# Kernel optimization log

Hardware: AMD Instinct MI355X
Metric: run time of the kernel (lower is better)

The kernel has to match this reference:

```python
import jax, jax.numpy as jnp
import numpy as np
import math

NUM_HEADS = 16
HEAD_DIM = 64
DIM = 1024
IO_SLOTS = 16
NEG_INF = 1.0e9


def _alibi_slopes(num_heads):
    # slopes = ratio**i for i in 1..n, ratio = 2**(-8/n)
    ratio = 2.0 ** (-8.0 / num_heads)
    return jnp.array([ratio ** i for i in range(1, num_heads + 1)], dtype=jnp.float32)


def setup_inputs() -> dict:
    key = jax.random.key(0)
    ks = jax.random.split(key, 7)
    B, S, D = 2, 2048, DIM
    x = jax.random.normal(ks[0], (B, S, D), dtype=jnp.float32)
    is_getchar = jax.random.uniform(ks[1], (B, S), dtype=jnp.float32)
    is_putchar = jax.random.uniform(ks[2], (B, S), dtype=jnp.float32)
    scale = 0.02
    wq = jax.random.normal(ks[3], (D, NUM_HEADS * HEAD_DIM), dtype=jnp.float32) * scale
    wk = jax.random.normal(ks[4], (D, NUM_HEADS * HEAD_DIM), dtype=jnp.float32) * scale
    wv = jax.random.normal(ks[5], (D, NUM_HEADS * HEAD_DIM), dtype=jnp.float32) * scale
    wo = jax.random.normal(ks[6], (NUM_HEADS * HEAD_DIM, D), dtype=jnp.float32) * scale
    return {"x": x, "is_getchar": is_getchar, "is_putchar": is_putchar,
            "wq": wq, "wk": wk, "wv": wv, "wo": wo}


def reference(x, is_getchar, is_putchar, wq, wk, wv, wo):
    B, S, D = x.shape
    H, hd = NUM_HEADS, HEAD_DIM
    io_start = D - IO_SLOTS

    q = (x @ wq).reshape(B, S, H, hd)
    k = (x @ wk).reshape(B, S, H, hd)
    v = (x @ wv).reshape(B, S, H, hd)

    # scores[b,h,i,j] = q . k / sqrt(hd)
    scores = jnp.einsum("bihd,bjhd->bhij", q, k) / math.sqrt(hd)

    # standard ALiBi bias: -slope * (i - j), causal masked
    positions = jnp.arange(S)
    dist = (positions[:, None] - positions[None, :]).astype(jnp.float32)  # [S,S] = i - j
    slopes = _alibi_slopes(H)  # [H]
    bias = -slopes[:, None, None] * dist  # [H,S,S]
    causal = jnp.triu(jnp.ones((S, S), dtype=jnp.float32), k=1)
    bias = bias - causal * NEG_INF
    scores = scores + bias[None]

    # targeted read-head bias on head 0: -slope0 * |target - j|
    read_anchor = x[..., io_start + 0]  # [B,S]
    read_offset = x[..., io_start + 1]  # [B,S]
    target = read_anchor + 1.0 + read_offset  # [B,S]
    read_bias = -slopes[0] * jnp.abs(target[..., None] - positions.astype(jnp.float32))  # [B,S,S]
    head0 = jnp.where(is_getchar[:, None, :, None] > 0.5, read_bias[:, None], scores[:, :1])
    scores = scores.at[:, :1].set(head0)

    attn = jax.nn.softmax(scores, axis=-1)
    attn_out = jnp.einsum("bhij,bjhd->bihd", attn, v).reshape(B, S, H * hd)
    output = x + attn_out @ wo

    # I/O state updates (last 16 channels)
    output = output.at[..., io_start + 1].add(is_getchar)   # read_offset += getchar
    output = output.at[..., io_start + 3].add(is_putchar)   # write_offset += putchar
    output = output.at[..., io_start + 13].set(is_putchar)  # output_ready = putchar
    return output
```

## Files before the change

kernel.cpp:

```cpp
#include <hip/hip_runtime.h>
#include <hip/hip_bf16.h>

typedef __hip_bfloat16 bf16;
typedef __attribute__((ext_vector_type(8))) short short8;
typedef __attribute__((ext_vector_type(4))) short short4v;
typedef __attribute__((ext_vector_type(4))) float f32x4;

#define MFMA16(a, b, c) __builtin_amdgcn_mfma_f32_16x16x32_bf16((a), (b), (c), 0, 0, 0)

#if __has_builtin(__builtin_amdgcn_mfma_f32_16x16x16bf16_1k)
#define MFMA_PV(a, b, c) __builtin_amdgcn_mfma_f32_16x16x16bf16_1k((a), (b), (c), 0, 0, 0)
#elif __has_builtin(__builtin_amdgcn_mfma_f32_16x16x16_bf16)
#define MFMA_PV(a, b, c) __builtin_amdgcn_mfma_f32_16x16x16_bf16((a), (b), (c), 0, 0, 0)
#else
static __device__ __forceinline__ f32x4 mfma_pv_asm(short4v a, short4v b, f32x4 c) {
    f32x4 d;
    asm volatile("v_mfma_f32_16x16x16_bf16 %0, %1, %2, %3"
                 : "=&v"(d) : "v"(a), "v"(b), "v"(c));
    return d;
}
#define MFMA_PV(a, b, c) mfma_pv_asm((a), (b), (c))
#endif

static __device__ __forceinline__ void gload_lds16(const bf16* g, bf16* l) {
    __builtin_amdgcn_global_load_lds((const __attribute__((address_space(1))) void*)g,
                                     (__attribute__((address_space(3))) void*)l, 16, 0, 0);
}

__global__ __launch_bounds__(256) void prep_kernel(
    const float* __restrict__ x, bf16* __restrict__ Xb,
    const float* __restrict__ wq, const float* __restrict__ wk,
    const float* __restrict__ wv, const float* __restrict__ wo,
    bf16* __restrict__ WqkvT, bf16* __restrict__ WoT) {
    __shared__ bf16 tile[64][65];
    int bidx = blockIdx.x;
    if (bidx >= 1024) {
        int i = ((bidx - 1024) * 256 + threadIdx.x) * 4;
        float4 v = *(const float4*)(x + i);
        union { bf16 h4[4]; uint2 u; } p;
        p.h4[0] = __float2bfloat16(v.x);
        p.h4[1] = __float2bfloat16(v.y);
        p.h4[2] = __float2bfloat16(v.z);
        p.h4[3] = __float2bfloat16(v.w);
        *(uint2*)(Xb + i) = p.u;
        return;
    }
    int mat = bidx >> 8;
    int t   = bidx & 255;
    int tn  = t >> 4, tk = t & 15;
    const float* src = (mat == 0) ? wq : (mat == 1) ? wk : (mat == 2) ? wv : wo;
    bf16* dst = (mat < 3) ? (WqkvT + (size_t)mat * 1024 * 1024) : WoT;
    int tx = threadIdx.x & 63, ty = threadIdx.x >> 6;
    int k0 = tk * 64, n0 = tn * 64;
#pragma unroll
    for (int p = 0; p < 16; ++p) {
        int r = p * 4 + ty;
        tile[r][tx] = __float2bfloat16(src[(size_t)(k0 + r) * 1024 + n0 + tx]);
    }
    __syncthreads();
#pragma unroll
    for (int p = 0; p < 16; ++p) {
        int r = p * 4 + ty;
        dst[(size_t)(n0 + r) * 1024 + k0 + tx] = tile[tx][r];
    }
}

__global__ __launch_bounds__(256) void gemm_qkv_kernel(
    const bf16* __restrict__ A, const bf16* __restrict__ Bt,
    bf16* __restrict__ QK, bf16* __restrict__ Vt) {
    const int K = 1024;
    int bm = blockIdx.x, bn = blockIdx.y;
    __shared__ bf16 As[128 * 32];
    __shared__ bf16 Bs[128 * 32];
    int tid = threadIdx.x;
    int lane = tid & 63, w = tid >> 6;
    int wm = (w >> 1) * 64, wn = (w & 1) * 64;
    int q4 = lane >> 4, li = lane & 15;
    int srow = tid >> 2, sc = (tid & 3) * 8;

    const bf16* Ag = A + (size_t)(bm * 128 + srow) * K + sc;
    const bf16* Bg = Bt + (size_t)(bn * 128 + srow) * K + sc;
    bf16* Asl = As + tid * 8;
    bf16* Asl2 = As + 2048 + tid * 8;
    bf16* Bsl = Bs + tid * 8;
    bf16* Bsl2 = Bs + 2048 + tid * 8;

    f32x4 acc[4][4];
#pragma unroll
    for (int mt = 0; mt < 4; ++mt)
#pragma unroll
        for (int nt = 0; nt < 4; ++nt) acc[mt][nt] = (f32x4){0.f, 0.f, 0.f, 0.f};

    for (int k0 = 0; k0 < K; k0 += 32) {
        __syncthreads();
        gload_lds16(Ag + k0, Asl);
        gload_lds16(Ag + 64 * K + k0, Asl2);
        gload_lds16(Bg + k0, Bsl);
        gload_lds16(Bg + 64 * K + k0, Bsl2);
        __syncthreads();
        short8 af[4], bfb[4];
#pragma unroll
        for (int mt = 0; mt < 4; ++mt)
            af[mt] = *(const short8*)(As + (wm + mt * 16 + li) * 32 + q4 * 8);
#pragma unroll
        for (int nt = 0; nt < 4; ++nt)
            bfb[nt] = *(const short8*)(Bs + (wn + nt * 16 + li) * 32 + q4 * 8);
#pragma unroll
        for (int mt = 0; mt < 4; ++mt)
#pragma unroll
            for (int nt = 0; nt < 4; ++nt)
                acc[mt][nt] = MFMA16(af[mt], bfb[nt], acc[mt][nt]);
    }

    int rowb = bm * 128 + wm;
    if (bn < 16) {
        float qs = (bn < 8) ? 0.1803368801111204f : 1.0f;
#pragma unroll
        for (int mt = 0; mt < 4; ++mt) {
#pragma unroll
            for (int nt = 0; nt < 4; ++nt) {
                int col = bn * 128 + wn + nt * 16 + li;
#pragma unroll
                for (int r = 0; r < 4; ++r) {
                    int row = rowb + mt * 16 + q4 * 4 + r;
                    QK[(size_t)row * 2048 + col] = __float2bfloat16(acc[mt][nt][r] * qs);
                }
            }
        }
    } else {
#pragma unroll
        for (int mt = 0; mt < 4; ++mt) {
            int sbase = rowb + mt * 16 + q4 * 4;
            int b = sbase >> 11, s = sbase & 2047;
#pragma unroll
            for (int nt = 0; nt < 4; ++nt) {
                int n = bn * 128 + wn + nt * 16 + li - 2048;
                int h = n >> 6, d = n & 63;
                union { bf16 h4[4]; uint2 u; } pk;
#pragma unroll
                for (int r = 0; r < 4; ++r) pk.h4[r] = __float2bfloat16(acc[mt][nt][r]);
                *(uint2*)(Vt + (size_t)((b * 16 + h) * 64 + d) * 2048 + s) = pk.u;
            }
        }
    }
}

__global__ __launch_bounds__(256, 3) void attn_kernel(
    const bf16* __restrict__ QK, const bf16* __restrict__ Vt,
    const float* __restrict__ x, const float* __restrict__ gch,
    bf16* __restrict__ AO) {
    const int S = 2048;
    int idx = blockIdx.x;
    int ti, h, b;
    if (idx < 64) { h = 0; b = idx & 1; ti = idx >> 1; }
    else {
        int i2 = idx - 64;
        int row = i2 / 30;
        int j = i2 - row * 30;
        ti = 31 - row; h = 1 + (j >> 1); b = j & 1;
    }
    int i0 = ti * 64;
    int tid = threadIdx.x, lane = tid & 63, w = tid >> 6;
    int q4 = lane >> 4, li = lane & 15;

    __shared__ __align__(16) char smem[36864];
    bf16* KsB = (bf16*)smem;
    bf16* VsB = (bf16*)(smem + 18432);
    float* Ored = (float*)smem;
    float* lsumBuf = (float*)(smem + 17408);

    short8 qf[4][2];
#pragma unroll
    for (int it = 0; it < 4; ++it) {
        const bf16* qp = QK + (size_t)(b * S + i0 + it * 16 + li) * 2048 + h * 64 + q4 * 8;
        qf[it][0] = *(const short8*)(qp);
        qf[it][1] = *(const short8*)(qp + 32);
    }

    const float L2E = 1.4426950408889634f;
    float slope = exp2f(-0.5f * (float)(h + 1));
    float sl1 = slope * L2E;
    const float slope0_1 = 0.70710678118654752f * L2E;

    float tgt[4]; int gcm[4];
    if (h == 0) {
#pragma unroll
        for (int it = 0; it < 4; ++it) {
            size_t ix = (size_t)(b * S + i0 + it * 16 + li);
            gcm[it] = gch[ix] > 0.5f ? 1 : 0;
            tgt[it] = x[ix * 1024 + 1008] + 1.0f + x[ix * 1024 + 1009];
        }
    } else {
#pragma unroll
        for (int it = 0; it < 4; ++it) { gcm[it] = 0; tgt[it] = 0.f; }
    }

    float lsum[4] = {0.f, 0.f, 0.f, 0.f};
    f32x4 o[4][4];
#pragma unroll
    for (int it = 0; it < 4; ++it)
#pragma unroll
        for (int dt = 0; dt < 4; ++dt) o[it][dt] = (f32x4){0.f, 0.f, 0.f, 0.f};

    int srow = tid >> 3, scv = (tid & 7) * 8;
    const bf16* Kg = QK + (size_t)(b * S + srow) * 2048 + 1024 + h * 64 + scv;
    const bf16* Vg = Vt + (size_t)((b * 16 + h) * 64 + srow) * 2048 + scv;

    int ntiles = (h == 0) ? (S / 64) : (ti + 1);

    {
        uint4 kv0 = *(const uint4*)(Kg);
        uint4 kv1 = *(const uint4*)(Kg + (size_t)32 * 2048);
        uint4 vv0 = *(const uint4*)(Vg);
        uint4 vv1 = *(const uint4*)(Vg + (size_t)32 * 2048);
        *(uint4*)(KsB + srow * 72 + scv) = kv0;
        *(uint4*)(KsB + (srow + 32) * 72 + scv) = kv1;
        *(uint4*)(VsB + srow * 72 + scv) = vv0;
        *(uint4*)(VsB + (srow + 32) * 72 + scv) = vv1;
    }
    __syncthreads();

    int cur = 0;
    for (int jt = 0; jt < ntiles; ++jt) {
        int j0 = jt * 64;
        uint4 nk0, nk1, nv0, nv1;
        bool pref = (jt + 1 < ntiles);
        if (pref) {
            int jn = j0 + 64;
            nk0 = *(const uint4*)(Kg + (size_t)jn * 2048);
            nk1 = *(const uint4*)(Kg + (size_t)(jn + 32) * 2048);
            nv0 = *(const uint4*)(Vg + jn);
            nv1 = *(const uint4*)(Vg + (size_t)32 * 2048 + jn);
        }
        const bf16* Ks = KsB + cur * 4608;
        const bf16* Vs = VsB + cur * 4608;

        short8 kf0 = *(const short8*)(Ks + (w * 16 + li) * 72 + q4 * 8);
        short8 kf1 = *(const short8*)(Ks + (w * 16 + li) * 72 + 32 + q4 * 8);
        f32x4 sAcc[4];
#pragma unroll
        for (int it = 0; it < 4; ++it) {
            f32x4 z = (f32x4){0.f, 0.f, 0.f, 0.f};
            z = MFMA16(kf0, qf[it][0], z);
            z = MFMA16(kf1, qf[it][1], z);
            sAcc[it] = z;
        }

        float jbase = (float)(j0 + w * 16 + q4 * 4);
        int maskable = (jt >= ti);
        short4v pf[4];
#pragma unroll
        for (int it = 0; it < 4; ++it) {
            float fi = (float)(i0 + it * 16 + li);
            float d0 = jbase - fi;
            union { bf16 hh[4]; short4v v; } pu;
#pragma unroll
            for (int r = 0; r < 4; ++r) {
                float dj = d0 + (float)r;
                float s = fmaf(sl1, dj, sAcc[it][r]);
                float p;
                if (h == 0) {
                    float jj = jbase + (float)r;
                    float sg = -slope0_1 * fabsf(tgt[it] - jj);
                    s = gcm[it] ? sg : s;
                    bool msk = (!gcm[it]) && (dj > 0.f);
                    p = msk ? 0.f : exp2f(s);
                } else {
                    p = exp2f(s);
                    if (maskable && dj > 0.f) p = 0.f;
                }
                lsum[it] += p;
                pu.hh[r] = __float2bfloat16(p);
            }
            pf[it] = pu.v;
        }

#pragma unroll
        for (int dt = 0; dt < 4; ++dt) {
            short4v vf = *(const short4v*)(Vs + (dt * 16 + li) * 72 + w * 16 + q4 * 4);
#pragma unroll
            for (int it = 0; it < 4; ++it)
                o[it][dt] = MFMA_PV(pf[it], vf, o[it][dt]);
        }

        if (pref) {
            bf16* Kn = KsB + (cur ^ 1) * 4608;
            bf16* Vn = VsB + (cur ^ 1) * 4608;
            *(uint4*)(Kn + srow * 72 + scv) = nk0;
            *(uint4*)(Kn + (srow + 32) * 72 + scv) = nk1;
            *(uint4*)(Vn + srow * 72 + scv) = nv0;
            *(uint4*)(Vn + (srow + 32) * 72 + scv) = nv1;
        }
        __syncthreads();
        cur ^= 1;
    }

#pragma unroll
    for (int it = 0; it < 4; ++it) {
        lsum[it] += __shfl_xor(lsum[it], 16, 64);
        lsum[it] += __shfl_xor(lsum[it], 32, 64);
    }
    if (lane < 16) {
#pragma unroll
        for (int it = 0; it < 4; ++it) lsumBuf[w * 64 + it * 16 + lane] = lsum[it];
    }

    __syncthreads();
    if (w == 0) {
#pragma unroll
        for (int it = 0; it < 4; ++it)
#pragma unroll
            for (int dt = 0; dt < 4; ++dt)
#pragma unroll
                for (int r = 0; r < 4; ++r)
                    Ored[(it * 16 + q4 * 4 + r) * 68 + dt * 16 + li] = o[it][dt][r];
    }
    __syncthreads();
    if (w == 1) {
#pragma unroll
        for (int it = 0; it < 4; ++it)
#pragma unroll
            for (int dt = 0; dt < 4; ++dt)
#pragma unroll
                for (int r = 0; r < 4; ++r)
                    Ored[(it * 16 + q4 * 4 + r) * 68 + dt * 16 + li] += o[it][dt][r];
    }
    __syncthreads();
    if (w == 2) {
#pragma unroll
        for (int it = 0; it < 4; ++it)
#pragma unroll
            for (int dt = 0; dt < 4; ++dt)
#pragma unroll
                for (int r = 0; r < 4; ++r)
                    Ored[(it * 16 + q4 * 4 + r) * 68 + dt * 16 + li] += o[it][dt][r];
    }
    __syncthreads();
    if (w == 3) {
#pragma unroll
        for (int it = 0; it < 4; ++it)
#pragma unroll
            for (int dt = 0; dt < 4; ++dt)
#pragma unroll
                for (int r = 0; r < 4; ++r)
                    Ored[(it * 16 + q4 * 4 + r) * 68 + dt * 16 + li] += o[it][dt][r];
    }
    __syncthreads();

    int i = tid >> 2, dseg = (tid & 3) * 16;
    float ls = lsumBuf[0 * 64 + i] + lsumBuf[1 * 64 + i] + lsumBuf[2 * 64 + i] + lsumBuf[3 * 64 + i];
    float inv = 1.0f / ls;
    bf16* dst = AO + (size_t)(b * S + i0 + i) * 1024 + h * 64 + dseg;
    union { bf16 hh[16]; uint4 u[2]; } ou;
#pragma unroll
    for (int c = 0; c < 16; ++c)
        ou.hh[c] = __float2bfloat16(Ored[i * 68 + dseg + c] * inv);
    *(uint4*)(dst) = ou.u[0];
    *(uint4*)(dst + 8) = ou.u[1];
}

__global__ __launch_bounds__(256) void gemm_out_kernel(
    const bf16* __restrict__ A, const bf16* __restrict__ Bt,
    const float* __restrict__ x, float* __restrict__ out,
    const float* __restrict__ gch, const float* __restrict__ pch) {
    const int K = 1024;
    int bm = blockIdx.x, bn = blockIdx.y;
    __shared__ bf16 As[64 * 32];
    __shared__ bf16 Bs[128 * 32];
    int tid = threadIdx.x;
    int lane = tid & 63, w = tid >> 6;
    int wm = (w >> 1) * 32, wn = (w & 1) * 64;
    int q4 = lane >> 4, li = lane & 15;
    int srow = tid >> 2, sc = (tid & 3) * 8;

    const bf16* Ag = A + (size_t)(bm * 64 + srow) * K + sc;
    const bf16* Bg = Bt + (size_t)(bn * 128 + srow) * K + sc;
    bf16* Asl = As + tid * 8;
    bf16* Bsl = Bs + tid * 8;
    bf16* Bsl2 = Bs + 2048 + tid * 8;

    f32x4 acc[2][4];
#pragma unroll
    for (int mt = 0; mt < 2; ++mt)
#pragma unroll
        for (int nt = 0; nt < 4; ++nt) acc[mt][nt] = (f32x4){0.f, 0.f, 0.f, 0.f};

    for (int k0 = 0; k0 < K; k0 += 32) {
        __syncthreads();
        gload_lds16(Ag + k0, Asl);
        gload_lds16(Bg + k0, Bsl);
        gload_lds16(Bg + 64 * K + k0, Bsl2);
        __syncthreads();
        short8 af[2], bfb[4];
#pragma unroll
        for (int mt = 0; mt < 2; ++mt)
            af[mt] = *(const short8*)(As + (wm + mt * 16 + li) * 32 + q4 * 8);
#pragma unroll
        for (int nt = 0; nt < 4; ++nt)
            bfb[nt] = *(const short8*)(Bs + (wn + nt * 16 + li) * 32 + q4 * 8);
#pragma unroll
        for (int mt = 0; mt < 2; ++mt)
#pragma unroll
            for (int nt = 0; nt < 4; ++nt)
                acc[mt][nt] = MFMA16(af[mt], bfb[nt], acc[mt][nt]);
    }

#pragma unroll
    for (int mt = 0; mt < 2; ++mt) {
#pragma unroll
        for (int nt = 0; nt < 4; ++nt) {
            int col = bn * 128 + wn + nt * 16 + li;
#pragma unroll
            for (int r = 0; r < 4; ++r) {
                int row = bm * 64 + wm + mt * 16 + q4 * 4 + r;
                size_t idx = (size_t)row * 1024 + col;
                float v = x[idx] + acc[mt][nt][r];
                if (col == 1009) v += gch[row];
                else if (col == 1011) v += pch[row];
                else if (col == 1021) v = pch[row];
                out[idx] = v;
            }
        }
    }
}

extern "C" void kernel_launch(void* const* d_in, const int* in_sizes, int n_in,
                              void* d_out, int out_size, void* d_ws, size_t ws_size,
                              hipStream_t stream) {
    (void)in_sizes; (void)n_in; (void)out_size; (void)ws_size;
    const float* x   = (const float*)d_in[0];
    const float* gch = (const float*)d_in[1];
    const float* pch = (const float*)d_in[2];
    const float* wq  = (const float*)d_in[3];
    const float* wk  = (const float*)d_in[4];
    const float* wv  = (const float*)d_in[5];
    const float* wo  = (const float*)d_in[6];
    float* out = (float*)d_out;

    char* ws = (char*)d_ws;
    bf16* Xb    = (bf16*)(ws);
    bf16* WqkvT = (bf16*)(ws + (size_t)( 8 << 20));
    bf16* WoT   = (bf16*)(ws + (size_t)(14 << 20));
    bf16* QK    = (bf16*)(ws + (size_t)(16 << 20));
    bf16* Vt    = (bf16*)(ws + (size_t)(32 << 20));
    bf16* AO    = Xb;

    prep_kernel<<<5120, 256, 0, stream>>>(x, Xb, wq, wk, wv, wo, WqkvT, WoT);
    gemm_qkv_kernel<<<dim3(32, 24), 256, 0, stream>>>(Xb, WqkvT, QK, Vt);
    attn_kernel<<<1024, 256, 0, stream>>>(QK, Vt, x, gch, AO);
    gemm_out_kernel<<<dim3(64, 8), 256, 0, stream>>>(AO, WoT, x, out, gch, pch);
}
```

Baseline: 198.7 us.

## Double QKV GEMM K-tile to 64 with XOR-swizzled LDS layout

The QKV projection GEMM now stages 64-wide K slices per iteration instead of 32, which halves the number of barrier pairs per K loop and issues more global-to-LDS loads per sync. The global source column is XOR-permuted by row so that the 128-byte LDS rows are swizzled, and the fragment reads apply the matching XOR to avoid bank conflicts. It doubles LDS use for this kernel, which may reduce occupancy.

```diff
diff --git a/kernel.cpp b/kernel.cpp
--- a/kernel.cpp
+++ b/kernel.cpp
@@ -70,20 +70,17 @@
     bf16* __restrict__ QK, bf16* __restrict__ Vt) {
     const int K = 1024;
     int bm = blockIdx.x, bn = blockIdx.y;
-    __shared__ bf16 As[128 * 32];
-    __shared__ bf16 Bs[128 * 32];
+    __shared__ bf16 As[128 * 64];
+    __shared__ bf16 Bs[128 * 64];
     int tid = threadIdx.x;
     int lane = tid & 63, w = tid >> 6;
     int wm = (w >> 1) * 64, wn = (w & 1) * 64;
     int q4 = lane >> 4, li = lane & 15;
-    int srow = tid >> 2, sc = (tid & 3) * 8;
-
-    const bf16* Ag = A + (size_t)(bm * 128 + srow) * K + sc;
-    const bf16* Bg = Bt + (size_t)(bn * 128 + srow) * K + sc;
-    bf16* Asl = As + tid * 8;
-    bf16* Asl2 = As + 2048 + tid * 8;
-    bf16* Bsl = Bs + tid * 8;
-    bf16* Bsl2 = Bs + 2048 + tid * 8;
+
+    int srow = tid >> 3;
+    int swc = ((tid & 7) ^ (srow & 7)) * 8;
+    const bf16* Ag = A + (size_t)(bm * 128 + srow) * K + swc;
+    const bf16* Bg = Bt + (size_t)(bn * 128 + srow) * K + swc;
 
     f32x4 acc[4][4];
 #pragma unroll
@@ -91,25 +88,33 @@
 #pragma unroll
         for (int nt = 0; nt < 4; ++nt) acc[mt][nt] = (f32x4){0.f, 0.f, 0.f, 0.f};
 
-    for (int k0 = 0; k0 < K; k0 += 32) {
+    int axr = (li & 7) * 8;
+
+    for (int k0 = 0; k0 < K; k0 += 64) {
         __syncthreads();
-        gload_lds16(Ag + k0, Asl);
-        gload_lds16(Ag + 64 * K + k0, Asl2);
-        gload_lds16(Bg + k0, Bsl);
-        gload_lds16(Bg + 64 * K + k0, Bsl2);
+#pragma unroll
+        for (int p = 0; p < 4; ++p) {
+            gload_lds16(Ag + (size_t)(p * 32) * K + k0, As + p * 2048 + tid * 8);
+            gload_lds16(Bg + (size_t)(p * 32) * K + k0, Bs + p * 2048 + tid * 8);
+        }
         __syncthreads();
-        short8 af[4], bfb[4];
-#pragma unroll
-        for (int mt = 0; mt < 4; ++mt)
-            af[mt] = *(const short8*)(As + (wm + mt * 16 + li) * 32 + q4 * 8);
-#pragma unroll
-        for (int nt = 0; nt < 4; ++nt)
-            bfb[nt] = *(const short8*)(Bs + (wn + nt * 16 + li) * 32 + q4 * 8);
-#pragma unroll
-        for (int mt = 0; mt < 4; ++mt)
+#pragma unroll
+        for (int kk = 0; kk < 2; ++kk) {
+            int lc = kk * 32 + q4 * 8;
+            int sc2 = lc ^ axr;
+            short8 af[4], bfb[4];
+#pragma unroll
+            for (int mt = 0; mt < 4; ++mt)
+                af[mt] = *(const short8*)(As + (wm + mt * 16 + li) * 64 + sc2);
 #pragma unroll
             for (int nt = 0; nt < 4; ++nt)
-                acc[mt][nt] = MFMA16(af[mt], bfb[nt], acc[mt][nt]);
+                bfb[nt] = *(const short8*)(Bs + (wn + nt * 16 + li) * 64 + sc2);
+#pragma unroll
+            for (int mt = 0; mt < 4; ++mt)
+#pragma unroll
+                for (int nt = 0; nt < 4; ++nt)
+                    acc[mt][nt] = MFMA16(af[mt], bfb[nt], acc[mt][nt]);
+        }
     }
 
     int rowb = bm * 128 + wm;
```

After: 204.6 us. 1.03x slower.
